# Kernel tuning notes

Measured on AMD Instinct MI355X. Metric: run time of the kernel, lower is better.

Reference implementation:

```python
import jax, jax.numpy as jnp
import numpy as np

N_NODES = 50000
N_EDGES = 1600000
IN_DIM = 128
OUT_DIM = 128
NEG_SLOPE = 0.01  # torch F.leaky_relu default


def setup_inputs() -> dict:
    key = jax.random.key(0)
    ks = jax.random.split(key, 8)
    feat = jax.random.normal(ks[0], (N_NODES, IN_DIM), dtype=jnp.float32)
    src = jax.random.randint(ks[1], (N_EDGES,), 0, N_NODES, dtype=jnp.int32)
    dst = jax.random.randint(ks[2], (N_EDGES,), 0, N_NODES, dtype=jnp.int32)
    W = jax.random.normal(ks[3], (IN_DIM, OUT_DIM), dtype=jnp.float32) / np.sqrt(IN_DIM)
    b = jax.random.normal(ks[4], (OUT_DIM,), dtype=jnp.float32) * 0.01
    attn_w = jax.random.normal(ks[5], (2 * OUT_DIM, 1), dtype=jnp.float32) / np.sqrt(2 * OUT_DIM)
    attn_b = jax.random.normal(ks[6], (1,), dtype=jnp.float32) * 0.01
    mask_weights = jnp.ones((IN_DIM,), dtype=jnp.float32)
    return {"feat": feat, "src": src, "dst": dst, "W": W, "b": b,
            "attn_w": attn_w, "attn_b": attn_b, "mask_weights": mask_weights}


def reference(feat, src, dst, W, b, attn_w, attn_b, mask_weights):
    N = feat.shape[0]
    d = W.shape[1]
    # feature masking + linear projection: [N, out_dim]
    h = (feat * jax.nn.sigmoid(mask_weights)) @ W + b
    # edge scores: attn_mlp(cat([h_src, h_dst])) split into two GEMVs to avoid
    # materializing the [E, 2d] concat
    s_src = (h @ attn_w[:d]).squeeze(-1)   # [N]
    s_dst = (h @ attn_w[d:]).squeeze(-1)   # [N]
    score = s_src[src] + s_dst[dst] + attn_b[0]          # [E]
    score = jnp.where(score >= 0, score, NEG_SLOPE * score)  # leaky_relu
    # segment softmax grouped by destination node (dgl.softmax over in-edges)
    mx = jax.ops.segment_max(score, dst, num_segments=N)     # [N]
    mx = jnp.where(jnp.isfinite(mx), mx, 0.0)                 # nodes w/o edges
    ex = jnp.exp(score - mx[dst])                             # [E]
    denom = jax.ops.segment_sum(ex, dst, num_segments=N)     # [N]
    a = ex / jnp.where(denom == 0, 1.0, denom)[dst]           # [E]
    # weighted scatter-sum: h_new[v] = sum_{(u,v) in E} a_uv * h[u]
    h_new = jax.ops.segment_sum(h[src] * a[:, None], dst, num_segments=N)
    return h_new
```

## Files before the change

### kernel.cpp

```cpp
#include <hip/hip_runtime.h>
#include <hip/hip_fp16.h>
#include <math.h>

#define N_NODES 50000
#define N_EDGES 1600000
#define NB 2000
#define NPB 25
#define NCH 100
#define EPC 16000
#define CAPC 32
#define CAP_LDS 1280
#define SPLIT 8
#define BPS (NB / SPLIT)
#define PLACE_BLOCKS (NCH * SPLIT)
#define PROJ_BLOCKS ((N_NODES + 31) / 32)

typedef _Float16 f16x8 __attribute__((ext_vector_type(8)));
typedef float f32x4 __attribute__((ext_vector_type(4)));


__global__ __launch_bounds__(256) void k_prep(const float* __restrict__ W,
                                              const float* __restrict__ b,
                                              const float* __restrict__ attn_w,
                                              __half* __restrict__ w16q,
                                              float* __restrict__ waSD,
                                              float* __restrict__ cst) {
    const int blk = blockIdx.x, t = threadIdx.x;
    if (blk < 8) {
        const int k = blk * 16 + (t >> 4), sub = t & 15;
        const float4* W4 = (const float4*)W;
        float4 w0 = W4[k * 32 + sub * 2];
        float4 w1 = W4[k * 32 + sub * 2 + 1];
        const int j0 = sub * 8;
        float pS = w0.x * attn_w[j0]     + w0.y * attn_w[j0 + 1]
                 + w0.z * attn_w[j0 + 2] + w0.w * attn_w[j0 + 3]
                 + w1.x * attn_w[j0 + 4] + w1.y * attn_w[j0 + 5]
                 + w1.z * attn_w[j0 + 6] + w1.w * attn_w[j0 + 7];
        float pD = w0.x * attn_w[128 + j0]     + w0.y * attn_w[128 + j0 + 1]
                 + w0.z * attn_w[128 + j0 + 2] + w0.w * attn_w[128 + j0 + 3]
                 + w1.x * attn_w[128 + j0 + 4] + w1.y * attn_w[128 + j0 + 5]
                 + w1.z * attn_w[128 + j0 + 6] + w1.w * attn_w[128 + j0 + 7];
        pS += __shfl_down(pS, 8); pS += __shfl_down(pS, 4);
        pS += __shfl_down(pS, 2); pS += __shfl_down(pS, 1);
        pD += __shfl_down(pD, 8); pD += __shfl_down(pD, 4);
        pD += __shfl_down(pD, 2); pD += __shfl_down(pD, 1);
        if (sub == 0) { waSD[k] = pS; waSD[128 + k] = pD; }
    } else if (blk < 40) {
        for (int e = (blk - 8) * 256 + t; e < 16384; e += 8192) {
            int j = e & 7, l = (e >> 3) & 63, kb = (e >> 9) & 3, ct = e >> 11;
            int k = kb * 32 + (l >> 4) * 8 + j;
            int c = ct * 16 + (l & 15);
            w16q[e] = __float2half(W[k * 128 + c]);
        }
    } else if (t < 64) {
        float vS = b[t] * attn_w[t]       + b[t + 64] * attn_w[t + 64];
        float vD = b[t] * attn_w[128 + t] + b[t + 64] * attn_w[192 + t];
        for (int off = 32; off; off >>= 1) {
            vS += __shfl_down(vS, off);
            vD += __shfl_down(vD, off);
        }
        if (t == 0) { cst[0] = vS; cst[1] = vD; }
    }
}

__global__ __launch_bounds__(512) void k_fusedA(const float* __restrict__ feat,
                                                const float* __restrict__ b,
                                                const float* __restrict__ mask,
                                                const int* __restrict__ src,
                                                const int* __restrict__ dst,
                                                __half* __restrict__ h16q,
                                                float* __restrict__ s_src,
                                                float* __restrict__ s_dst,
                                                int* __restrict__ cnt,
                                                unsigned* __restrict__ gep,
                                                const __half* __restrict__ w16q,
                                                const float* __restrict__ waSD,
                                                const float* __restrict__ cst) {
    __shared__ __align__(16) char smem[33024];
    const int blk = blockIdx.x;
    const int t = threadIdx.x;

    if (blk < PLACE_BLOCKS) {
        int* cur = (int*)smem;
        unsigned* lcell = (unsigned*)(smem + 1024);
        const int c = blk >> 3, sp = blk & 7;
        const int b0 = sp * BPS;
        for (int i = t; i < BPS; i += 512) cur[i] = 0;
        __syncthreads();
        const int q0 = c * (EPC / 4);
        for (int q = t; q < EPC / 4; q += 512) {
            int4 s4 = ((const int4*)src)[q0 + q];
            int4 d4 = ((const int4*)dst)[q0 + q];
            int ss[4] = {s4.x, s4.y, s4.z, s4.w};
            int dd[4] = {d4.x, d4.y, d4.z, d4.w};
#pragma unroll
            for (int k = 0; k < 4; k++) {
                int d = dd[k];
                int bkt = d / NPB;
                if (bkt >= b0 && bkt < b0 + BPS) {
                    int dl = d - bkt * NPB;
                    int lb = bkt - b0;
                    int r = atomicAdd(&cur[lb], 1);
                    if (r < CAPC)
                        lcell[lb * CAPC + r] = ((unsigned)ss[k] << 5) | (unsigned)dl;
                }
            }
        }
        __syncthreads();
        const uint4* lc4 = (const uint4*)lcell;
        uint4* gp4 = (uint4*)gep;
        for (int idx = t; idx < BPS * (CAPC / 4); idx += 512) {
            int i = idx >> 3, q = idx & 7;
            gp4[((size_t)(b0 + i) * NCH + c) * 8 + q] = lc4[idx];
        }
        for (int i = t; i < BPS; i += 512) cnt[c * NB + b0 + i] = min(cur[i], CAPC);
    } else {
        float* sAW = (float*)(smem + 8192);
        float* sAD = (float*)(smem + 8704);
        float* sig = (float*)(smem + 9216);
        const int bb = blk - PLACE_BLOCKS;
        const int row0 = bb * 32;
        if (t < 128) {
            sig[t] = 1.f / (1.f + expf(-mask[t]));
            sAW[t] = waSD[t];
            sAD[t] = waSD[128 + t];
        }
        __syncthreads();
        for (int idx = t; idx < 32 * 32; idx += 512) {
            int r = idx >> 5, c4 = idx & 31;
            int grow = row0 + r;
            float4 f;
            if (grow < N_NODES) f = ((const float4*)feat)[grow * 32 + c4];
            else f = make_float4(0.f, 0.f, 0.f, 0.f);
            int c = c4 * 4;
            ushort4 pk;
            pk.x = __half_as_ushort(__float2half(f.x * sig[c]));
            pk.y = __half_as_ushort(__float2half(f.y * sig[c + 1]));
            pk.z = __half_as_ushort(__float2half(f.z * sig[c + 2]));
            pk.w = __half_as_ushort(__float2half(f.w * sig[c + 3]));
            int byte = (r * 256 + c4 * 8) ^ ((r & 7) << 4);
            *(ushort4*)(smem + byte) = pk;
        }
        __syncthreads();
        const int wv = t >> 6, l = t & 63;
        const int lr = l & 15, lk = l >> 4;
        const f16x8* wq = (const f16x8*)w16q;
        f32x4 acc0 = {0.f, 0.f, 0.f, 0.f};
        f32x4 acc1 = {0.f, 0.f, 0.f, 0.f};
#pragma unroll
        for (int kb = 0; kb < 4; kb++) {
            f16x8 Bf = wq[(wv * 4 + kb) * 64 + l];
            int co = kb * 64 + lk * 16;
            f16x8 A0 = *(const f16x8*)(smem + ((lr * 256 + co) ^ ((lr & 7) << 4)));
            f16x8 A1 = *(const f16x8*)(smem + (((16 + lr) * 256 + co) ^ ((lr & 7) << 4)));
            acc0 = __builtin_amdgcn_mfma_f32_16x16x32_f16(A0, Bf, acc0, 0, 0, 0);
            acc1 = __builtin_amdgcn_mfma_f32_16x16x32_f16(A1, Bf, acc1, 0, 0, 0);
        }
        {
            const int r2 = t >> 4, sub = t & 15;
            f16x8 xv = *(const f16x8*)(smem + ((r2 * 256 + sub * 16) ^ ((r2 & 7) << 4)));
            float ss = 0.f, sd = 0.f;
#pragma unroll
            for (int q = 0; q < 8; q++) {
                float v = (float)xv[q];
                int jj = sub * 8 + q;
                ss = fmaf(v, sAW[jj], ss);
                sd = fmaf(v, sAD[jj], sd);
            }
            ss += __shfl_down(ss, 8); ss += __shfl_down(ss, 4);
            ss += __shfl_down(ss, 2); ss += __shfl_down(ss, 1);
            sd += __shfl_down(sd, 8); sd += __shfl_down(sd, 4);
            sd += __shfl_down(sd, 2); sd += __shfl_down(sd, 1);
            int grow = row0 + r2;
            if (sub == 0 && grow < N_NODES) {
                s_src[grow] = ss + cst[0];
                s_dst[grow] = sd + cst[1];
            }
        }
        const float bj = b[wv * 16 + lr];
        __half* hp = h16q + (size_t)(wv >> 1) * (N_NODES * 32) + ((wv & 1) * 16 + lr);
#pragma unroll
        for (int reg = 0; reg < 4; reg++) {
            int n0 = row0 + lk * 4 + reg;
            if (n0 < N_NODES) hp[(size_t)n0 * 32] = __float2half(acc0[reg] + bj);
            int n1 = n0 + 16;
            if (n1 < N_NODES) hp[(size_t)n1 * 32] = __float2half(acc1[reg] + bj);
        }
    }
}

__global__ __launch_bounds__(256) void k_sort(const float* __restrict__ s_src,
                                              const float* __restrict__ s_dst,
                                              const float* __restrict__ attn_b,
                                              const int* __restrict__ cnt,
                                              unsigned* gep,
                                              int* __restrict__ rp_g) {
    __shared__ unsigned raw[CAP_LDS];
    __shared__ unsigned srt[CAP_LDS];
    __shared__ float wbuf[CAP_LDS];
    __shared__ int ccnt[NCH];
    __shared__ int coff[NCH];
    __shared__ int hist[NPB];
    __shared__ int rp[NPB + 1];
    __shared__ int curn[NPB];
    __shared__ float sdl[NPB];
    __shared__ float dsum[NPB];
    __shared__ float dinv[NPB];
    __shared__ int totsh;
    const int bkt = blockIdx.x;
    const int t = threadIdx.x;
    if (t < NCH) ccnt[t] = cnt[t * NB + bkt];
    if (t < NPB) { hist[t] = 0; dsum[t] = 0.f; sdl[t] = s_dst[bkt * NPB + t]; }
    __syncthreads();
    if (t < 64) {
        int i0 = 2 * t, i1 = 2 * t + 1;
        int a0 = (i0 < NCH) ? ccnt[i0] : 0;
        int a1 = (i1 < NCH) ? ccnt[i1] : 0;
        int s = a0 + a1, incl = s;
#pragma unroll
        for (int off = 1; off < 64; off <<= 1) {
            int v = __shfl_up(incl, off);
            if (t >= off) incl += v;
        }
        int excl = incl - s;
        if (i0 < NCH) coff[i0] = excl;
        if (i1 < NCH) coff[i1] = excl + a0;
        if (t == 63) totsh = incl;
    }
    __syncthreads();
    int total = totsh;
    if (total > CAP_LDS) total = CAP_LDS;
    unsigned* gb = gep + (size_t)bkt * (NCH * CAPC);
    for (int i = t; i < NCH * CAPC; i += 256) {
        unsigned e = gb[i];
        int cell = i >> 5, slot = i & 31;
        if (slot < ccnt[cell]) {
            int pos = coff[cell] + slot;
            if (pos < CAP_LDS) {
                raw[pos] = e;
                atomicAdd(&hist[e & 31], 1);
            }
        }
    }
    __syncthreads();
    if (t == 0) {
        int run = 0;
        for (int j = 0; j < NPB; j++) { rp[j] = run; curn[j] = run; run += hist[j]; }
        rp[NPB] = run;
    }
    __syncthreads();
    const float ab = attn_b[0];
    for (int i = t; i < total; i += 256) {
        unsigned e = raw[i];
        int dl = e & 31;
        int s = (int)(e >> 5);
        float sc = s_src[s] + sdl[dl] + ab;
        sc = sc >= 0.f ? sc : 0.01f * sc;
        float w = expf(sc);
        int pos = atomicAdd(&curn[dl], 1);
        srt[pos] = ((unsigned)s << 16) | (unsigned)dl;
        wbuf[pos] = w;
        atomicAdd(&dsum[dl], w);
    }
    __syncthreads();
    if (t < NPB) dinv[t] = dsum[t] > 0.f ? 1.f / dsum[t] : 0.f;
    __syncthreads();
    for (int i = t; i < total; i += 256) {
        unsigned e = srt[i];
        float a = wbuf[i] * dinv[e & 31];
        gb[i] = (e & 0xFFFF0000u) | (unsigned)__half_as_ushort(__float2half(a));
    }
    if (t <= NPB) rp_g[bkt * 32 + t] = rp[t];
}

__device__ __forceinline__ void accum4(float4& a, uint2 u, float w) {
    __half2 p0 = *(const __half2*)&u.x;
    __half2 p1 = *(const __half2*)&u.y;
    float2 f0 = __half22float2(p0), f1 = __half22float2(p1);
    a.x = fmaf(w, f0.x, a.x); a.y = fmaf(w, f0.y, a.y);
    a.z = fmaf(w, f1.x, a.z); a.w = fmaf(w, f1.y, a.w);
}

__device__ __forceinline__ float wdec(unsigned e) {
    return __half2float(__ushort_as_half((unsigned short)(e & 0xFFFFu)));
}

__global__ __launch_bounds__(256) void k_gather(const __half* __restrict__ h16q,
                                                const unsigned* __restrict__ gep,
                                                const int* __restrict__ rp_g,
                                                float* __restrict__ out) {
    __shared__ int rp[NPB + 1];
    __shared__ unsigned se[CAP_LDS];
    const int blk = blockIdx.x;
    const int x = blk & 7;
    const int qq = x & 3;
    const int bkt = ((blk >> 3) << 1) + (x >> 2);
    const int t = threadIdx.x;
    if (t <= NPB) rp[t] = rp_g[bkt * 32 + t];
    __syncthreads();
    const int total = rp[NPB];
    const unsigned* sb = gep + (size_t)bkt * (NCH * CAPC);
    for (int i = t; i < total; i += 256) se[i] = sb[i];
    __syncthreads();
    const int wv = t >> 6, lane = t & 63;
    const int eg = lane >> 3;
    const int dp = lane & 7;
    const uint2* hq = (const uint2*)h16q + (size_t)qq * (N_NODES * 8) + dp;
    for (int n = wv; n < NPB; n += 4) {
        int lo = rp[n], hi = rp[n + 1];
        float4 a4 = {0.f, 0.f, 0.f, 0.f};
        for (int i = lo + eg; i < hi; i += 32) {
            unsigned e0 = se[i];
            unsigned e1 = (i + 8  < hi) ? se[i + 8]  : 0u;
            unsigned e2 = (i + 16 < hi) ? se[i + 16] : 0u;
            unsigned e3 = (i + 24 < hi) ? se[i + 24] : 0u;
            uint2 u0 = hq[(e0 >> 16) * 8];
            uint2 u1 = hq[(e1 >> 16) * 8];
            uint2 u2 = hq[(e2 >> 16) * 8];
            uint2 u3 = hq[(e3 >> 16) * 8];
            accum4(a4, u0, wdec(e0));
            accum4(a4, u1, wdec(e1));
            accum4(a4, u2, wdec(e2));
            accum4(a4, u3, wdec(e3));
        }
        a4.x += __shfl_xor(a4.x, 8); a4.x += __shfl_xor(a4.x, 16); a4.x += __shfl_xor(a4.x, 32);
        a4.y += __shfl_xor(a4.y, 8); a4.y += __shfl_xor(a4.y, 16); a4.y += __shfl_xor(a4.y, 32);
        a4.z += __shfl_xor(a4.z, 8); a4.z += __shfl_xor(a4.z, 16); a4.z += __shfl_xor(a4.z, 32);
        a4.w += __shfl_xor(a4.w, 8); a4.w += __shfl_xor(a4.w, 16); a4.w += __shfl_xor(a4.w, 32);
        if (eg == 0) {
            ((float4*)out)[(size_t)(bkt * NPB + n) * 32 + qq * 8 + dp] = a4;
        }
    }
}

extern "C" void kernel_launch(void* const* d_in, const int* in_sizes, int n_in,
                              void* d_out, int out_size, void* d_ws, size_t ws_size,
                              hipStream_t stream) {
    const float* feat   = (const float*)d_in[0];
    const int*   src    = (const int*)d_in[1];
    const int*   dst    = (const int*)d_in[2];
    const float* W      = (const float*)d_in[3];
    const float* b      = (const float*)d_in[4];
    const float* attn_w = (const float*)d_in[5];
    const float* attn_b = (const float*)d_in[6];
    const float* mask   = (const float*)d_in[7];
    float* out = (float*)d_out;

    char* ws = (char*)d_ws;
    __half*   h16q  = (__half*)(ws + 0);
    float*    s_src = (float*)(ws + 12800000);
    float*    s_dst = (float*)(ws + 13000000);
    int*      cnt   = (int*)(ws + 13200000);
    unsigned* gep   = (unsigned*)(ws + 14000000);
    int*      rp_g  = (int*)(ws + 39600000);
    __half*   w16q  = (__half*)(ws + 39856000);
    float*    waSD  = (float*)(ws + 39888768);
    float*    cst   = (float*)(ws + 39889792);

    k_prep<<<41, 256, 0, stream>>>(W, b, attn_w, w16q, waSD, cst);
    k_fusedA<<<PLACE_BLOCKS + PROJ_BLOCKS, 512, 0, stream>>>(
        feat, b, mask, src, dst, h16q, s_src, s_dst, cnt, gep, w16q, waSD, cst);
    k_sort<<<NB, 256, 0, stream>>>(s_src, s_dst, attn_b, cnt, gep, rp_g);
    k_gather<<<NB * 4, 256, 0, stream>>>(h16q, gep, rp_g, out);
}
```

Baseline: 186.0 us.

## Restructure gather kernel to one node per 4-lane group over 5 buckets

The gather kernel now makes each 512-thread block handle five destination buckets. Each 4-thread group owns one destination node and loads 16-byte fp16 chunks per lane, replacing the earlier scheme where 8 edge-groups shared a node and reduced through cross-lane shuffles. This removes the shuffle reductions and the wasted lanes on low-degree nodes, and widens the per-lane loads. In exchange, each thread walks the edges serially, so load balance depends on the degree distribution. 500 of the 512 threads are active, and LDS use per block is higher.

```diff
diff --git a/kernel.cpp b/kernel.cpp
--- a/kernel.cpp
+++ b/kernel.cpp
@@ -14,6 +14,9 @@
 #define BPS (NB / SPLIT)
 #define PLACE_BLOCKS (NCH * SPLIT)
 #define PROJ_BLOCKS ((N_NODES + 31) / 32)
+#define NBG 5
+#define NGRP (NBG * NPB)
+#define GQ_BLOCKS ((NB / (NBG * 2)) * 8)
 
 typedef _Float16 f16x8 __attribute__((ext_vector_type(8)));
 typedef float f32x4 __attribute__((ext_vector_type(4)));
@@ -273,63 +276,69 @@
     if (t <= NPB) rp_g[bkt * 32 + t] = rp[t];
 }
 
-__device__ __forceinline__ void accum4(float4& a, uint2 u, float w) {
+__device__ __forceinline__ void accum8(float4& A, float4& B, uint4 u, float w) {
     __half2 p0 = *(const __half2*)&u.x;
     __half2 p1 = *(const __half2*)&u.y;
+    __half2 p2 = *(const __half2*)&u.z;
+    __half2 p3 = *(const __half2*)&u.w;
     float2 f0 = __half22float2(p0), f1 = __half22float2(p1);
-    a.x = fmaf(w, f0.x, a.x); a.y = fmaf(w, f0.y, a.y);
-    a.z = fmaf(w, f1.x, a.z); a.w = fmaf(w, f1.y, a.w);
+    float2 f2 = __half22float2(p2), f3 = __half22float2(p3);
+    A.x = fmaf(w, f0.x, A.x); A.y = fmaf(w, f0.y, A.y);
+    A.z = fmaf(w, f1.x, A.z); A.w = fmaf(w, f1.y, A.w);
+    B.x = fmaf(w, f2.x, B.x); B.y = fmaf(w, f2.y, B.y);
+    B.z = fmaf(w, f3.x, B.z); B.w = fmaf(w, f3.y, B.w);
 }
 
 __device__ __forceinline__ float wdec(unsigned e) {
     return __half2float(__ushort_as_half((unsigned short)(e & 0xFFFFu)));
 }
 
-__global__ __launch_bounds__(256) void k_gather(const __half* __restrict__ h16q,
+__global__ __launch_bounds__(512) void k_gather(const __half* __restrict__ h16q,
                                                 const unsigned* __restrict__ gep,
                                                 const int* __restrict__ rp_g,
                                                 float* __restrict__ out) {
-    __shared__ int rp[NPB + 1];
-    __shared__ unsigned se[CAP_LDS];
+    __shared__ unsigned se[NBG * CAP_LDS];
+    __shared__ int rp[NBG * 32];
     const int blk = blockIdx.x;
     const int x = blk & 7;
     const int qq = x & 3;
-    const int bkt = ((blk >> 3) << 1) + (x >> 2);
+    const int bg = ((blk >> 3) << 1) + (x >> 2);
+    const int bkt0 = bg * NBG;
     const int t = threadIdx.x;
-    if (t <= NPB) rp[t] = rp_g[bkt * 32 + t];
-    __syncthreads();
-    const int total = rp[NPB];
-    const unsigned* sb = gep + (size_t)bkt * (NCH * CAPC);
-    for (int i = t; i < total; i += 256) se[i] = sb[i];
-    __syncthreads();
-    const int wv = t >> 6, lane = t & 63;
-    const int eg = lane >> 3;
-    const int dp = lane & 7;
-    const uint2* hq = (const uint2*)h16q + (size_t)qq * (N_NODES * 8) + dp;
-    for (int n = wv; n < NPB; n += 4) {
-        int lo = rp[n], hi = rp[n + 1];
-        float4 a4 = {0.f, 0.f, 0.f, 0.f};
-        for (int i = lo + eg; i < hi; i += 32) {
-            unsigned e0 = se[i];
-            unsigned e1 = (i + 8  < hi) ? se[i + 8]  : 0u;
-            unsigned e2 = (i + 16 < hi) ? se[i + 16] : 0u;
-            unsigned e3 = (i + 24 < hi) ? se[i + 24] : 0u;
-            uint2 u0 = hq[(e0 >> 16) * 8];
-            uint2 u1 = hq[(e1 >> 16) * 8];
-            uint2 u2 = hq[(e2 >> 16) * 8];
-            uint2 u3 = hq[(e3 >> 16) * 8];
-            accum4(a4, u0, wdec(e0));
-            accum4(a4, u1, wdec(e1));
-            accum4(a4, u2, wdec(e2));
-            accum4(a4, u3, wdec(e3));
-        }
-        a4.x += __shfl_xor(a4.x, 8); a4.x += __shfl_xor(a4.x, 16); a4.x += __shfl_xor(a4.x, 32);
-        a4.y += __shfl_xor(a4.y, 8); a4.y += __shfl_xor(a4.y, 16); a4.y += __shfl_xor(a4.y, 32);
-        a4.z += __shfl_xor(a4.z, 8); a4.z += __shfl_xor(a4.z, 16); a4.z += __shfl_xor(a4.z, 32);
-        a4.w += __shfl_xor(a4.w, 8); a4.w += __shfl_xor(a4.w, 16); a4.w += __shfl_xor(a4.w, 32);
-        if (eg == 0) {
-            ((float4*)out)[(size_t)(bkt * NPB + n) * 32 + qq * 8 + dp] = a4;
-        }
+    if (t < NBG * 32 && (t & 31) <= NPB)
+        rp[t] = rp_g[(bkt0 + (t >> 5)) * 32 + (t & 31)];
+    __syncthreads();
+#pragma unroll
+    for (int b = 0; b < NBG; b++) {
+        const unsigned* gb = gep + (size_t)(bkt0 + b) * (NCH * CAPC);
+        const int tot = rp[b * 32 + NPB];
+        for (int i = t; i < tot; i += 512) se[b * CAP_LDS + i] = gb[i];
+    }
+    __syncthreads();
+    const int g = t >> 2, dp = t & 3;
+    if (g < NGRP) {
+        const int b = g / NPB, n = g - b * NPB;
+        const int lo = rp[b * 32 + n], hi = rp[b * 32 + n + 1];
+        const unsigned* seb = se + b * CAP_LDS;
+        const uint4* hq = (const uint4*)h16q + (size_t)qq * (N_NODES * 4) + dp;
+        float4 A = {0.f, 0.f, 0.f, 0.f}, B = {0.f, 0.f, 0.f, 0.f};
+        for (int i = lo; i < hi; i += 4) {
+            unsigned e0 = seb[i];
+            unsigned e1 = (i + 1 < hi) ? seb[i + 1] : 0u;
+            unsigned e2 = (i + 2 < hi) ? seb[i + 2] : 0u;
+            unsigned e3 = (i + 3 < hi) ? seb[i + 3] : 0u;
+            uint4 u0 = hq[(e0 >> 16) * 4];
+            uint4 u1 = hq[(e1 >> 16) * 4];
+            uint4 u2 = hq[(e2 >> 16) * 4];
+            uint4 u3 = hq[(e3 >> 16) * 4];
+            accum8(A, B, u0, wdec(e0));
+            accum8(A, B, u1, wdec(e1));
+            accum8(A, B, u2, wdec(e2));
+            accum8(A, B, u3, wdec(e3));
+        }
+        float4* o = (float4*)(out + (size_t)(bg * 125 + g) * 128 + qq * 32 + dp * 8);
+        o[0] = A;
+        o[1] = B;
     }
 }
 
@@ -361,5 +370,5 @@
     k_fusedA<<<PLACE_BLOCKS + PROJ_BLOCKS, 512, 0, stream>>>(
         feat, b, mask, src, dst, h16q, s_src, s_dst, cnt, gep, w16q, waSD, cst);
     k_sort<<<NB, 256, 0, stream>>>(s_src, s_dst, attn_b, cnt, gep, rp_g);
-    k_gather<<<NB * 4, 256, 0, stream>>>(h16q, gep, rp_g, out);
-}
+    k_gather<<<GQ_BLOCKS, 512, 0, stream>>>(h16q, gep, rp_g, out);
+}
```

Result: faster. 176.5 us (-5.1%).
